# Kernel tuning notes

Hardware: AMD Instinct MI355X
Metric: run time of the kernel (lower is better)

Reference implementation:

```python
import jax, jax.numpy as jnp
import numpy as np

B, T, D, H = 8, 1024, 1024, 16
NEG = -1e9  # stands in for -inf in the causal mask (matches float('-inf') semantics under softmax)


def setup_inputs() -> dict:
    key = jax.random.key(0)
    ks = jax.random.split(key, 8)
    s = 0.02
    x = jax.random.normal(ks[0], (B, T, D), dtype=jnp.float32)
    # additive causal mask like whisper: zeros on/below diagonal, -inf above
    mask = jnp.triu(jnp.full((T, T), NEG, dtype=jnp.float32), k=1)
    Wq = jax.random.normal(ks[1], (D, D), dtype=jnp.float32) * s
    bq = jax.random.normal(ks[2], (D,), dtype=jnp.float32) * s
    Wk = jax.random.normal(ks[3], (D, D), dtype=jnp.float32) * s
    Wv = jax.random.normal(ks[4], (D, D), dtype=jnp.float32) * s
    bv = jax.random.normal(ks[5], (D,), dtype=jnp.float32) * s
    Wo = jax.random.normal(ks[6], (D, D), dtype=jnp.float32) * s
    bo = jax.random.normal(ks[7], (D,), dtype=jnp.float32) * s
    return {"x": x, "mask": mask, "Wq": Wq, "bq": bq, "Wk": Wk, "Wv": Wv, "bv": bv, "Wo": Wo, "bo": bo}


def reference(x, mask, Wq, bq, Wk, Wv, bv, Wo, bo):
    n_batch, n_ctx, n_state = x.shape
    head_dim = n_state // H
    scale = head_dim ** (-0.25)

    q = x @ Wq.T + bq            # [B,T,D]
    k = x @ Wk.T                 # key Linear has no bias
    v = x @ Wv.T + bv

    # [B,T,D] -> [B,H,T,hd]
    q = q.reshape(n_batch, n_ctx, H, head_dim).transpose(0, 2, 1, 3) * scale
    kt = k.reshape(n_batch, n_ctx, H, head_dim).transpose(0, 2, 3, 1) * scale  # [B,H,hd,T]
    v = v.reshape(n_batch, n_ctx, H, head_dim).transpose(0, 2, 1, 3)

    qk = jnp.einsum('bhqd,bhdk->bhqk', q, kt) + mask[:n_ctx, :n_ctx]
    w = jax.nn.softmax(qk.astype(jnp.float32), axis=-1).astype(q.dtype)
    wv = jnp.einsum('bhqk,bhkd->bhqd', w, v)  # [B,H,T,hd]
    wv = wv.transpose(0, 2, 1, 3).reshape(n_batch, n_ctx, n_state)
    return wv @ Wo.T + bo
```

## Files before the change

### kernel.cpp

```cpp
#include <hip/hip_runtime.h>
#include <stdint.h>

typedef unsigned short u16;
typedef __attribute__((ext_vector_type(8))) short bf16x8;
typedef __attribute__((ext_vector_type(4))) float f32x4;

__device__ __forceinline__ float b2f(u16 u) {
    union { uint32_t i; float f; } c; c.i = ((uint32_t)u) << 16; return c.f;
}
__device__ __forceinline__ u16 f2b(float f) {
    union { float f; uint32_t i; } c; c.f = f;
    uint32_t u = c.i;
    uint32_t r = (u + 0x7fffu + ((u >> 16) & 1u)) >> 16;
    return (u16)r;
}
__device__ __forceinline__ uint32_t fbits(float f) {
    union { float f; uint32_t u; } c; c.f = f; return c.u;
}

__device__ __forceinline__ void gll16(const u16* g, u16* lds_base) {
    __builtin_amdgcn_global_load_lds(
        (const __attribute__((address_space(1))) uint32_t*)g,
        (__attribute__((address_space(3))) uint32_t*)lds_base, 16, 0, 0);
}

#define GK 1024
#define QSCALE 0.18033688011112042f

__global__ __launch_bounds__(256) void conv_all(
    const void* x, const void* wq, const void* bqp, const void* wk,
    const void* wv, const void* bvp, const void* wo, const void* bop,
    u16* xb, u16* wqb, u16* bqb, u16* wkb, u16* wvb, u16* bvb, u16* wob, u16* bob,
    const u16* __restrict__ sniff)
{
    const bool is_f32 = (sniff[1] == 0);
    const int blk = blockIdx.x;
    const void* s; u16* d; int i0, n;
    if (blk < 4096)      { s = x;   d = xb;  i0 = blk;        n = 8388608; }
    else if (blk < 4608) { s = wq;  d = wqb; i0 = blk - 4096; n = 1048576; }
    else if (blk < 5120) { s = wk;  d = wkb; i0 = blk - 4608; n = 1048576; }
    else if (blk < 5632) { s = wv;  d = wvb; i0 = blk - 5120; n = 1048576; }
    else if (blk < 6144) { s = wo;  d = wob; i0 = blk - 5632; n = 1048576; }
    else if (blk == 6144){ s = bqp; d = bqb; i0 = 0;          n = 1024; }
    else if (blk == 6145){ s = bvp; d = bvb; i0 = 0;          n = 1024; }
    else                 { s = bop; d = bob; i0 = 0;          n = 1024; }
    int i = (i0 * 256 + threadIdx.x) * 8;
    if (i >= n) return;
    if (is_f32) {
        const float* sf = (const float*)s;
        float4 lo = *(const float4*)(sf + i);
        float4 hi = *(const float4*)(sf + i + 4);
        u16 o[8];
        o[0]=f2b(lo.x); o[1]=f2b(lo.y); o[2]=f2b(lo.z); o[3]=f2b(lo.w);
        o[4]=f2b(hi.x); o[5]=f2b(hi.y); o[6]=f2b(hi.z); o[7]=f2b(hi.w);
        *(uint4*)(d + i) = *(const uint4*)o;
    } else {
        *(uint4*)(d + i) = *(const uint4*)((const u16*)s + i);
    }
}

__global__ __launch_bounds__(256) void gemm_qkv(
    const u16* __restrict__ xb,
    const u16* __restrict__ wq, const u16* __restrict__ wk, const u16* __restrict__ wv,
    const u16* __restrict__ bq, const u16* __restrict__ bv,
    u16* __restrict__ qb, u16* __restrict__ kb, u16* __restrict__ vtb)
{
    __shared__ __align__(16) u16 As[128 * 64];
    __shared__ __align__(16) u16 Bs[128 * 64];

    const int flat = blockIdx.x;
    const int xcd = flat & 7, pos = flat >> 3;
    const int m0 = (xcd * 8 + (pos & 7)) * 128;
    const int nb = pos >> 3;
    const int which = nb >> 3;
    const int n0 = (nb & 7) * 128;
    const u16* W = (which == 0) ? wq : (which == 1) ? wk : wv;

    const int t = threadIdx.x;
    const int lane = t & 63, w = t >> 6;
    const int quad = lane >> 4, l15 = lane & 15;
    const int wm = (w >> 1) * 64, wn = (w & 1) * 64;
    const int srow = (lane >> 3), scol = (lane & 7) * 8;

    f32x4 acc[4][4];
#pragma unroll
    for (int i = 0; i < 4; i++)
#pragma unroll
        for (int j = 0; j < 4; j++)
            acc[i][j] = (f32x4){0.f, 0.f, 0.f, 0.f};

    for (int kk = 0; kk < GK / 64; kk++) {
        const int k0 = kk * 64;
        __syncthreads();
#pragma unroll
        for (int i = 0; i < 4; i++) {
            const int rbase = w * 32 + i * 8;
            gll16(xb + (size_t)(m0 + rbase + srow) * GK + k0 + scol, &As[rbase * 64]);
            gll16(W  + (size_t)(n0 + rbase + srow) * GK + k0 + scol, &Bs[rbase * 64]);
        }
        __syncthreads();
#pragma unroll
        for (int ks = 0; ks < 2; ks++) {
            bf16x8 af[4], bfr[4];
#pragma unroll
            for (int mi = 0; mi < 4; mi++)
                af[mi] = *(const bf16x8*)(&As[(wm + mi * 16 + l15) * 64 + ks * 32 + quad * 8]);
#pragma unroll
            for (int ni = 0; ni < 4; ni++)
                bfr[ni] = *(const bf16x8*)(&Bs[(wn + ni * 16 + l15) * 64 + ks * 32 + quad * 8]);
#pragma unroll
            for (int mi = 0; mi < 4; mi++)
#pragma unroll
                for (int ni = 0; ni < 4; ni++)
                    acc[mi][ni] = __builtin_amdgcn_mfma_f32_16x16x32_bf16(
                        af[mi], bfr[ni], acc[mi][ni], 0, 0, 0);
        }
    }

#pragma unroll
    for (int mi = 0; mi < 4; mi++)
#pragma unroll
        for (int ni = 0; ni < 4; ni++) {
            int gn = n0 + wn + ni * 16 + l15;
            if (which == 2) {
                int gmb = m0 + wm + mi * 16 + quad * 4;
                int b = gmb >> 10, ml = gmb & 1023;
                int h = gn >> 6, dw = gn & 63;
                union { u16 h4[4]; uint2 v; } pk;
#pragma unroll
                for (int r = 0; r < 4; r++)
                    pk.h4[r] = f2b(acc[mi][ni][r] + b2f(bv[gn]));
                *(uint2*)(vtb + (((size_t)(b * 16 + h) * 64 + dw) << 10) + ml) = pk.v;
            } else if (which == 0) {
                float bb = b2f(bq[gn]);
#pragma unroll
                for (int r = 0; r < 4; r++) {
                    int gm = m0 + wm + mi * 16 + quad * 4 + r;
                    qb[(size_t)gm * 1024 + gn] = f2b((acc[mi][ni][r] + bb) * QSCALE);
                }
            } else {
#pragma unroll
                for (int r = 0; r < 4; r++) {
                    int gm = m0 + wm + mi * 16 + quad * 4 + r;
                    kb[(size_t)gm * 1024 + gn] = f2b(acc[mi][ni][r]);
                }
            }
        }
}

__global__ __launch_bounds__(256) void gemm_out(
    const u16* __restrict__ A, const u16* __restrict__ W,
    const u16* __restrict__ bias, float* __restrict__ C)
{
    __shared__ __align__(16) u16 As[128 * 64];
    __shared__ __align__(16) u16 Bs[128 * 64];

    const int flat = blockIdx.x;
    const int xcd = flat & 7, pos = flat >> 3;
    const int m0 = (xcd * 8 + (pos & 7)) * 128;
    const int n0 = (pos >> 3) * 128;

    const int t = threadIdx.x;
    const int lane = t & 63, w = t >> 6;
    const int quad = lane >> 4, l15 = lane & 15;
    const int wm = (w >> 1) * 64, wn = (w & 1) * 64;
    const int srow = (lane >> 3), scol = (lane & 7) * 8;

    f32x4 acc[4][4];
#pragma unroll
    for (int i = 0; i < 4; i++)
#pragma unroll
        for (int j = 0; j < 4; j++)
            acc[i][j] = (f32x4){0.f, 0.f, 0.f, 0.f};

    for (int kk = 0; kk < GK / 64; kk++) {
        const int k0 = kk * 64;
        __syncthreads();
#pragma unroll
        for (int i = 0; i < 4; i++) {
            const int rbase = w * 32 + i * 8;
            gll16(A + (size_t)(m0 + rbase + srow) * GK + k0 + scol, &As[rbase * 64]);
            gll16(W + (size_t)(n0 + rbase + srow) * GK + k0 + scol, &Bs[rbase * 64]);
        }
        __syncthreads();
#pragma unroll
        for (int ks = 0; ks < 2; ks++) {
            bf16x8 af[4], bfr[4];
#pragma unroll
            for (int mi = 0; mi < 4; mi++)
                af[mi] = *(const bf16x8*)(&As[(wm + mi * 16 + l15) * 64 + ks * 32 + quad * 8]);
#pragma unroll
            for (int ni = 0; ni < 4; ni++)
                bfr[ni] = *(const bf16x8*)(&Bs[(wn + ni * 16 + l15) * 64 + ks * 32 + quad * 8]);
#pragma unroll
            for (int mi = 0; mi < 4; mi++)
#pragma unroll
                for (int ni = 0; ni < 4; ni++)
                    acc[mi][ni] = __builtin_amdgcn_mfma_f32_16x16x32_bf16(
                        af[mi], bfr[ni], acc[mi][ni], 0, 0, 0);
        }
    }

#pragma unroll
    for (int mi = 0; mi < 4; mi++)
#pragma unroll
        for (int ni = 0; ni < 4; ni++) {
            int gn = n0 + wn + ni * 16 + l15;
            float bb = b2f(bias[gn]);
#pragma unroll
            for (int r = 0; r < 4; r++) {
                int gm = m0 + wm + mi * 16 + quad * 4 + r;
                C[(size_t)gm * 1024 + gn] = acc[mi][ni][r] + bb;
            }
        }
}

__global__ __launch_bounds__(512) void attn_kernel(
    const u16* q, const u16* kg, const u16* vt, u16* o)
{
    const int qt = blockIdx.x;
    const int bh = blockIdx.y;
    const int b = bh >> 4, h = bh & 15;
    const size_t base = (size_t)b * 1024 * 1024 + (size_t)h * 64;
    const size_t vbase = (size_t)bh * 64 * 1024;

    __shared__ __align__(16) u16 Ks[64 * 72];
    __shared__ __align__(16) u16 Vs[64 * 72];
    __shared__ __align__(16) u16 U[128 * 72];

    const int t = threadIdx.x;
    const int lane = t & 63, w = t >> 6;
    const int quad = lane >> 4, l15 = lane & 15;

#pragma unroll
    for (int i = 0; i < 2; i++) {
        int idx = i * 512 + t;
        int r = idx >> 3, c = idx & 7;
        *(uint4*)(&U[r * 72 + c * 8]) =
            *(const uint4*)(q + base + (size_t)(qt * 128 + r) * 1024 + c * 8);
    }
    __syncthreads();
    const bf16x8 qf0 = *(const bf16x8*)(&U[(w * 16 + l15) * 72 + quad * 8]);
    const bf16x8 qf1 = *(const bf16x8*)(&U[(w * 16 + l15) * 72 + 32 + quad * 8]);
    __syncthreads();
    u16* Pw = &U[(w * 16) * 72];

    const int wqmin = qt * 128 + w * 16;
    const int q_g = wqmin + l15;
    float l_ = 0.f;
    f32x4 accO[4];
#pragma unroll
    for (int f = 0; f < 4; f++) accO[f] = (f32x4){0.f, 0.f, 0.f, 0.f};

    const int jmax = 2 * qt + 1;
    const int sr = t >> 3, sc = (t & 7) * 8;
    uint4 rK = *(const uint4*)(kg + base + (size_t)sr * 1024 + sc);
    uint4 rV = *(const uint4*)(vt + vbase + (size_t)sr * 1024 + sc);

    for (int j = 0; j <= jmax; j++) {
        __syncthreads();
        *(uint4*)(&Ks[sr * 72 + sc]) = rK;
        *(uint4*)(&Vs[sr * 72 + sc]) = rV;
        __syncthreads();
        if (j < jmax) {
            rK = *(const uint4*)(kg + base + (size_t)((j + 1) * 64 + sr) * 1024 + sc);
            rV = *(const uint4*)(vt + vbase + (size_t)sr * 1024 + (j + 1) * 64 + sc);
        }
        if (j * 64 > wqmin + 15) continue;

        f32x4 st[4];
#pragma unroll
        for (int ni = 0; ni < 4; ni++) st[ni] = (f32x4){0.f, 0.f, 0.f, 0.f};
#pragma unroll
        for (int ks = 0; ks < 2; ks++) {
            bf16x8 qf = ks ? qf1 : qf0;
#pragma unroll
            for (int ni = 0; ni < 4; ni++) {
                bf16x8 kf = *(const bf16x8*)(&Ks[(ni * 16 + l15) * 72 + ks * 32 + quad * 8]);
                st[ni] = __builtin_amdgcn_mfma_f32_16x16x32_bf16(kf, qf, st[ni], 0, 0, 0);
            }
        }

        const bool diag = (j * 64 + 63 > wqmin);
        float ps = 0.f;
#pragma unroll
        for (int ni = 0; ni < 4; ni++) {
            float p[4];
#pragma unroll
            for (int r = 0; r < 4; r++) {
                float e = __builtin_amdgcn_exp2f(st[ni][r]);
                if (diag) {
                    int key_g = j * 64 + ni * 16 + quad * 4 + r;
                    e = (key_g > q_g) ? 0.f : e;
                }
                p[r] = e;
                ps += e;
            }
            uint2 pkv;
            pkv.x = __builtin_amdgcn_perm(fbits(p[1]) + 0x8000u, fbits(p[0]) + 0x8000u, 0x07060302u);
            pkv.y = __builtin_amdgcn_perm(fbits(p[3]) + 0x8000u, fbits(p[2]) + 0x8000u, 0x07060302u);
            *(uint2*)(&Pw[l15 * 72 + ni * 16 + quad * 4]) = pkv;
        }
        l_ += ps;

#pragma unroll
        for (int ks = 0; ks < 2; ks++) {
            bf16x8 pf = *(const bf16x8*)(&Pw[l15 * 72 + ks * 32 + quad * 8]);
#pragma unroll
            for (int f = 0; f < 4; f++) {
                bf16x8 vf = *(const bf16x8*)(&Vs[(f * 16 + l15) * 72 + ks * 32 + quad * 8]);
                accO[f] = __builtin_amdgcn_mfma_f32_16x16x32_bf16(vf, pf, accO[f], 0, 0, 0);
            }
        }
    }

    l_ += __shfl_xor(l_, 16, 64);
    l_ += __shfl_xor(l_, 32, 64);
    float inv = 1.0f / l_;
#pragma unroll
    for (int f = 0; f < 4; f++) {
        union { u16 h4[4]; uint2 v; } pk;
#pragma unroll
        for (int r = 0; r < 4; r++) pk.h4[r] = f2b(accO[f][r] * inv);
        *(uint2*)(o + base + (size_t)q_g * 1024 + f * 16 + quad * 4) = pk.v;
    }
}

extern "C" void kernel_launch(void* const* d_in, const int* in_sizes, int n_in,
                              void* d_out, int out_size, void* d_ws, size_t ws_size,
                              hipStream_t stream) {
    const u16* mask = (const u16*)d_in[1];

    const size_t MT = (size_t)8192 * 1024;
    const size_t WT = (size_t)1024 * 1024;
    u16* ws  = (u16*)d_ws;
    u16* xb  = ws;
    u16* qb  = xb + MT;
    u16* kb  = qb + MT;
    u16* vtb = kb + MT;
    u16* wqb = vtb + MT;
    u16* wkb = wqb + WT;
    u16* wvb = wkb + WT;
    u16* wob = wvb + WT;
    u16* bqb = wob + WT;
    u16* bvb = bqb + 1024;
    u16* bob = bvb + 1024;

    hipLaunchKernelGGL(conv_all, dim3(6147), dim3(256), 0, stream,
                       d_in[0], d_in[2], d_in[3], d_in[4], d_in[5], d_in[6],
                       d_in[7], d_in[8],
                       xb, wqb, bqb, wkb, wvb, bvb, wob, bob, mask);

    hipLaunchKernelGGL(gemm_qkv, dim3(1536), dim3(256), 0, stream,
                       xb, wqb, wkb, wvb, bqb, bvb, qb, kb, vtb);

    hipLaunchKernelGGL(attn_kernel, dim3(8, 128), dim3(512), 0, stream, qb, kb, vtb, qb);

    hipLaunchKernelGGL(gemm_out, dim3(512), dim3(256), 0, stream,
                       qb, wob, bob, (float*)d_out);
}
```

Baseline: 275.6 us.

## Enlarge attention query tile to 256 rows with double-buffered K/V LDS

The attention kernel now processes 256 query rows per block instead of 128. Each wave owns two 16-row query chunks, so every K/V fragment read from LDS feeds two MFMAs. K/V staging is double-buffered, which drops one barrier per key-tile iteration. The query-tile index is also permuted across heads to mix causal work lengths, and launch bounds are tightened. The trade-offs are half as many blocks, more register pressure and more LDS per block, which may leave CUs underfilled and worsen causal load imbalance.

```diff
diff --git a/kernel.cpp b/kernel.cpp
--- a/kernel.cpp
+++ b/kernel.cpp
@@ -26,6 +26,7 @@
 
 #define GK 1024
 #define QSCALE 0.18033688011112042f
+#define LDPA 72
 
 __global__ __launch_bounds__(256) void conv_all(
     const void* x, const void* wq, const void* bqp, const void* wk,
@@ -215,114 +216,132 @@
         }
 }
 
-__global__ __launch_bounds__(512) void attn_kernel(
+__global__ __launch_bounds__(512, 4) void attn_kernel(
     const u16* q, const u16* kg, const u16* vt, u16* o)
 {
-    const int qt = blockIdx.x;
+    const int qt = (blockIdx.x + 2 * (blockIdx.y >> 6)) & 3;
     const int bh = blockIdx.y;
     const int b = bh >> 4, h = bh & 15;
     const size_t base = (size_t)b * 1024 * 1024 + (size_t)h * 64;
     const size_t vbase = (size_t)bh * 64 * 1024;
 
-    __shared__ __align__(16) u16 Ks[64 * 72];
-    __shared__ __align__(16) u16 Vs[64 * 72];
-    __shared__ __align__(16) u16 U[128 * 72];
+    __shared__ __align__(16) u16 Ks[2][64 * LDPA];
+    __shared__ __align__(16) u16 Vs[2][64 * LDPA];
+    __shared__ __align__(16) u16 U[256 * LDPA];
 
     const int t = threadIdx.x;
     const int lane = t & 63, w = t >> 6;
     const int quad = lane >> 4, l15 = lane & 15;
 
 #pragma unroll
-    for (int i = 0; i < 2; i++) {
+    for (int i = 0; i < 4; i++) {
         int idx = i * 512 + t;
         int r = idx >> 3, c = idx & 7;
-        *(uint4*)(&U[r * 72 + c * 8]) =
-            *(const uint4*)(q + base + (size_t)(qt * 128 + r) * 1024 + c * 8);
+        *(uint4*)(&U[r * LDPA + c * 8]) =
+            *(const uint4*)(q + base + (size_t)(qt * 256 + r) * 1024 + c * 8);
     }
     __syncthreads();
-    const bf16x8 qf0 = *(const bf16x8*)(&U[(w * 16 + l15) * 72 + quad * 8]);
-    const bf16x8 qf1 = *(const bf16x8*)(&U[(w * 16 + l15) * 72 + 32 + quad * 8]);
+    bf16x8 qf[2][2];
+#pragma unroll
+    for (int qc = 0; qc < 2; qc++)
+#pragma unroll
+        for (int ks = 0; ks < 2; ks++)
+            qf[qc][ks] = *(const bf16x8*)(&U[(w * 32 + qc * 16 + l15) * LDPA + ks * 32 + quad * 8]);
     __syncthreads();
-    u16* Pw = &U[(w * 16) * 72];
-
-    const int wqmin = qt * 128 + w * 16;
-    const int q_g = wqmin + l15;
-    float l_ = 0.f;
-    f32x4 accO[4];
-#pragma unroll
-    for (int f = 0; f < 4; f++) accO[f] = (f32x4){0.f, 0.f, 0.f, 0.f};
-
-    const int jmax = 2 * qt + 1;
+    u16* Pw = &U[(w * 32) * LDPA];
+
+    const int wqmin = qt * 256 + w * 32;
+    float l_[2] = {0.f, 0.f};
+    f32x4 accO[2][4];
+#pragma unroll
+    for (int qc = 0; qc < 2; qc++)
+#pragma unroll
+        for (int f = 0; f < 4; f++) accO[qc][f] = (f32x4){0.f, 0.f, 0.f, 0.f};
+
+    const int jmax = 4 * qt + 3;
     const int sr = t >> 3, sc = (t & 7) * 8;
     uint4 rK = *(const uint4*)(kg + base + (size_t)sr * 1024 + sc);
     uint4 rV = *(const uint4*)(vt + vbase + (size_t)sr * 1024 + sc);
 
     for (int j = 0; j <= jmax; j++) {
-        __syncthreads();
-        *(uint4*)(&Ks[sr * 72 + sc]) = rK;
-        *(uint4*)(&Vs[sr * 72 + sc]) = rV;
-        __syncthreads();
+        const int buf = j & 1;
+        *(uint4*)(&Ks[buf][sr * LDPA + sc]) = rK;
+        *(uint4*)(&Vs[buf][sr * LDPA + sc]) = rV;
         if (j < jmax) {
             rK = *(const uint4*)(kg + base + (size_t)((j + 1) * 64 + sr) * 1024 + sc);
             rV = *(const uint4*)(vt + vbase + (size_t)sr * 1024 + (j + 1) * 64 + sc);
         }
-        if (j * 64 > wqmin + 15) continue;
-
-        f32x4 st[4];
-#pragma unroll
-        for (int ni = 0; ni < 4; ni++) st[ni] = (f32x4){0.f, 0.f, 0.f, 0.f};
+        __syncthreads();
+
+        if (j * 64 > wqmin + 31) continue;
+
+        f32x4 st[2][4];
+#pragma unroll
+        for (int qc = 0; qc < 2; qc++)
+#pragma unroll
+            for (int ni = 0; ni < 4; ni++) st[qc][ni] = (f32x4){0.f, 0.f, 0.f, 0.f};
+#pragma unroll
+        for (int ks = 0; ks < 2; ks++)
+#pragma unroll
+            for (int ni = 0; ni < 4; ni++) {
+                bf16x8 kf = *(const bf16x8*)(&Ks[buf][(ni * 16 + l15) * LDPA + ks * 32 + quad * 8]);
+                st[0][ni] = __builtin_amdgcn_mfma_f32_16x16x32_bf16(kf, qf[0][ks], st[0][ni], 0, 0, 0);
+                st[1][ni] = __builtin_amdgcn_mfma_f32_16x16x32_bf16(kf, qf[1][ks], st[1][ni], 0, 0, 0);
+            }
+
+        const bool diag = (j * 64 + 63 > wqmin);
+#pragma unroll
+        for (int qc = 0; qc < 2; qc++) {
+            const int q_g = wqmin + qc * 16 + l15;
+            float ps = 0.f;
+#pragma unroll
+            for (int ni = 0; ni < 4; ni++) {
+                float p[4];
+#pragma unroll
+                for (int r = 0; r < 4; r++) {
+                    float e = __builtin_amdgcn_exp2f(st[qc][ni][r]);
+                    if (diag) {
+                        int key_g = j * 64 + ni * 16 + quad * 4 + r;
+                        e = (key_g > q_g) ? 0.f : e;
+                    }
+                    p[r] = e;
+                    ps += e;
+                }
+                uint2 pkv;
+                pkv.x = __builtin_amdgcn_perm(fbits(p[1]) + 0x8000u, fbits(p[0]) + 0x8000u, 0x07060302u);
+                pkv.y = __builtin_amdgcn_perm(fbits(p[3]) + 0x8000u, fbits(p[2]) + 0x8000u, 0x07060302u);
+                *(uint2*)(&Pw[(qc * 16 + l15) * LDPA + ni * 16 + quad * 4]) = pkv;
+            }
+            l_[qc] += ps;
+        }
+
 #pragma unroll
         for (int ks = 0; ks < 2; ks++) {
-            bf16x8 qf = ks ? qf1 : qf0;
-#pragma unroll
-            for (int ni = 0; ni < 4; ni++) {
-                bf16x8 kf = *(const bf16x8*)(&Ks[(ni * 16 + l15) * 72 + ks * 32 + quad * 8]);
-                st[ni] = __builtin_amdgcn_mfma_f32_16x16x32_bf16(kf, qf, st[ni], 0, 0, 0);
-            }
-        }
-
-        const bool diag = (j * 64 + 63 > wqmin);
-        float ps = 0.f;
-#pragma unroll
-        for (int ni = 0; ni < 4; ni++) {
-            float p[4];
-#pragma unroll
-            for (int r = 0; r < 4; r++) {
-                float e = __builtin_amdgcn_exp2f(st[ni][r]);
-                if (diag) {
-                    int key_g = j * 64 + ni * 16 + quad * 4 + r;
-                    e = (key_g > q_g) ? 0.f : e;
-                }
-                p[r] = e;
-                ps += e;
-            }
-            uint2 pkv;
-            pkv.x = __builtin_amdgcn_perm(fbits(p[1]) + 0x8000u, fbits(p[0]) + 0x8000u, 0x07060302u);
-            pkv.y = __builtin_amdgcn_perm(fbits(p[3]) + 0x8000u, fbits(p[2]) + 0x8000u, 0x07060302u);
-            *(uint2*)(&Pw[l15 * 72 + ni * 16 + quad * 4]) = pkv;
-        }
-        l_ += ps;
-
-#pragma unroll
-        for (int ks = 0; ks < 2; ks++) {
-            bf16x8 pf = *(const bf16x8*)(&Pw[l15 * 72 + ks * 32 + quad * 8]);
+            bf16x8 pf0 = *(const bf16x8*)(&Pw[(l15) * LDPA + ks * 32 + quad * 8]);
+            bf16x8 pf1 = *(const bf16x8*)(&Pw[(16 + l15) * LDPA + ks * 32 + quad * 8]);
 #pragma unroll
             for (int f = 0; f < 4; f++) {
-                bf16x8 vf = *(const bf16x8*)(&Vs[(f * 16 + l15) * 72 + ks * 32 + quad * 8]);
-                accO[f] = __builtin_amdgcn_mfma_f32_16x16x32_bf16(vf, pf, accO[f], 0, 0, 0);
-            }
-        }
-    }
-
-    l_ += __shfl_xor(l_, 16, 64);
-    l_ += __shfl_xor(l_, 32, 64);
-    float inv = 1.0f / l_;
-#pragma unroll
-    for (int f = 0; f < 4; f++) {
-        union { u16 h4[4]; uint2 v; } pk;
-#pragma unroll
-        for (int r = 0; r < 4; r++) pk.h4[r] = f2b(accO[f][r] * inv);
-        *(uint2*)(o + base + (size_t)q_g * 1024 + f * 16 + quad * 4) = pk.v;
+                bf16x8 vf = *(const bf16x8*)(&Vs[buf][(f * 16 + l15) * LDPA + ks * 32 + quad * 8]);
+                accO[0][f] = __builtin_amdgcn_mfma_f32_16x16x32_bf16(vf, pf0, accO[0][f], 0, 0, 0);
+                accO[1][f] = __builtin_amdgcn_mfma_f32_16x16x32_bf16(vf, pf1, accO[1][f], 0, 0, 0);
+            }
+        }
+    }
+
+#pragma unroll
+    for (int qc = 0; qc < 2; qc++) {
+        float l = l_[qc];
+        l += __shfl_xor(l, 16, 64);
+        l += __shfl_xor(l, 32, 64);
+        float inv = 1.0f / l;
+        const int q_g = wqmin + qc * 16 + l15;
+#pragma unroll
+        for (int f = 0; f < 4; f++) {
+            union { u16 h4[4]; uint2 v; } pk;
+#pragma unroll
+            for (int r = 0; r < 4; r++) pk.h4[r] = f2b(accO[qc][f][r] * inv);
+            *(uint2*)(o + base + (size_t)q_g * 1024 + f * 16 + quad * 4) = pk.v;
+        }
     }
 }
 
@@ -354,7 +373,7 @@
     hipLaunchKernelGGL(gemm_qkv, dim3(1536), dim3(256), 0, stream,
                        xb, wqb, wkb, wvb, bqb, bvb, qb, kb, vtb);
 
-    hipLaunchKernelGGL(attn_kernel, dim3(8, 128), dim3(512), 0, stream, qb, kb, vtb, qb);
+    hipLaunchKernelGGL(attn_kernel, dim3(4, 128), dim3(512), 0, stream, qb, kb, vtb, qb);
 
     hipLaunchKernelGGL(gemm_out, dim3(512), dim3(256), 0, stream,
                        qb, wob, bob, (float*)d_out);
```

Measured after the change: 255.4 us. -7.3%, faster.
